# Optimization experiments

Measured on AMD Instinct MI355X. Metric: run time of the kernel, lower is better.

## Reference

```python
import jax, jax.numpy as jnp
import numpy as np

HEAD_SIZE = 64
NUM_HEADS = 8
D_IN = 512

def setup_inputs() -> dict:
    key = jax.random.key(0)
    ks = jax.random.split(key, 6)
    B, Nq, Nk = 4, 2048, 2048
    HD = HEAD_SIZE * NUM_HEADS
    q = jax.random.normal(ks[0], (B, Nq, D_IN), dtype=jnp.float32)
    k = jax.random.normal(ks[1], (B, Nk, D_IN), dtype=jnp.float32)
    s = 1.0 / np.sqrt(D_IN)
    Wq = jax.random.normal(ks[2], (D_IN, HD), dtype=jnp.float32) * s
    Wk = jax.random.normal(ks[3], (D_IN, HD), dtype=jnp.float32) * s
    Wv = jax.random.normal(ks[4], (D_IN, HD), dtype=jnp.float32) * s
    Wh = jax.random.normal(ks[5], (HD, HEAD_SIZE), dtype=jnp.float32) * (1.0 / np.sqrt(HD))
    return {"q": q, "k": k, "Wq": Wq, "Wk": Wk, "Wv": Wv, "Wh": Wh}

def reference(q, k, Wq, Wk, Wv, Wh):
    B, Nq, _ = q.shape
    Nk = k.shape[1]
    H, hs = NUM_HEADS, HEAD_SIZE
    # QKV projections (no bias), reshape to [B, H, N, hs]
    q_ = (q @ Wq).reshape(B, Nq, H, hs).transpose(0, 2, 1, 3)
    k_ = (k @ Wk).reshape(B, Nk, H, hs).transpose(0, 2, 1, 3)
    v_ = (k @ Wv).reshape(B, Nk, H, hs).transpose(0, 2, 1, 3)
    scale = 1.0 / jnp.sqrt(jnp.float32(hs))
    score = jnp.einsum('bhqd,bhkd->bhqk', q_, k_) * scale  # [B,H,Nq,Nk]
    attn = jax.nn.softmax(score, axis=-1)
    wv = jnp.einsum('bhqk,bhkd->bhqd', attn, v_)  # [B,H,Nq,hs]
    wv = wv.transpose(0, 2, 1, 3).reshape(B, Nq, H * hs)
    return wv @ Wh  # [B, Nq, hs]
```

## Files before the change

kernel.cpp:

```cpp
#include <hip/hip_runtime.h>
#include <hip/hip_bf16.h>

#define BB   4
#define NQ   2048
#define NKK  2048
#define DIN  512
#define NH   8
#define HS   64
#define HD   512

typedef __hip_bfloat16 bf16;
typedef unsigned short ushort_t;
typedef __attribute__((ext_vector_type(8))) short short8;
typedef __attribute__((ext_vector_type(4))) float f32x4;
typedef __attribute__((ext_vector_type(16))) float f32x16;
typedef __attribute__((ext_vector_type(4))) unsigned u32x4;

__device__ __forceinline__ unsigned short f2bu(float x) {
  bf16 h = __float2bfloat16(x);
  return *(unsigned short*)&h;
}

__global__ __launch_bounds__(256) void wtrans_kernel(
    const float* __restrict__ Wq, const float* __restrict__ Wk,
    const float* __restrict__ Wv, const float* __restrict__ Wh,
    ushort_t* __restrict__ Wt, ushort_t* __restrict__ Wht) {
  const int z = blockIdx.z;
  const float* src;
  ushort_t* dst;
  int S;
  if (z < 3) {
    src = (z == 0) ? Wq : (z == 1) ? Wk : Wv;
    dst = Wt + (size_t)z * 512 * 512;
    S = 512;
  } else {
    if (blockIdx.y != 0) return;
    src = Wh;
    dst = Wht;
    S = 64;
  }
  const int k0 = blockIdx.x * 64;
  const int n0 = (z < 3) ? blockIdx.y * 64 : 0;

  __shared__ ushort_t Ls[64 * 72];
  const int tid = threadIdx.x;
  {
    int r = tid >> 2, cb = (tid & 3) * 16;
    const float* sp = src + (size_t)(k0 + r) * S + n0 + cb;
#pragma unroll
    for (int ii = 0; ii < 4; ++ii) {
      float4 f = *(const float4*)(sp + ii * 4);
      __align__(8) ushort_t t4[4] = {f2bu(f.x), f2bu(f.y), f2bu(f.z), f2bu(f.w)};
      *(uint2*)(&Ls[r * 72 + cb + ii * 4]) = *(uint2*)t4;
    }
  }
  __syncthreads();
  {
    int rr = tid >> 2, tb = (tid & 3) * 16;
    __align__(16) ushort_t tmp[16];
#pragma unroll
    for (int j = 0; j < 16; ++j) tmp[j] = Ls[(tb + j) * 72 + rr];
    ushort_t* dp = dst + (size_t)(n0 + rr) * 512 + k0 + tb;
    *(int4*)dp       = ((int4*)tmp)[0];
    *(int4*)(dp + 8) = ((int4*)tmp)[1];
  }
}

__global__ __launch_bounds__(256) void proj_kernel(
    const float* __restrict__ q, const float* __restrict__ k,
    const ushort_t* __restrict__ Wt, ushort_t* __restrict__ Qf,
    ushort_t* __restrict__ Kf, ushort_t* __restrict__ Vf) {
  const int z = blockIdx.z;
  const float* X = (z == 0) ? q : k;
  const ushort_t* Wz = Wt + (size_t)z * 512 * 512;
  ushort_t* Y = (z == 0) ? Qf : (z == 1) ? Kf : Vf;
  const float sc = (z == 0) ? 0.18033688011112042f : 1.0f;

  __shared__ ushort_t As[2 * 128 * 40];
  __shared__ ushort_t Bs[2 * 128 * 40];

  const int tid  = threadIdx.x;
  const int lane = tid & 63;
  const int w    = tid >> 6;
  const int quad = lane >> 4;
  const int c    = lane & 15;
  const int wm   = w >> 1, wn = w & 1;

  const int m0 = blockIdx.y * 128;
  const int n0 = blockIdx.x * 128;
  const int sm  = tid >> 1;
  const int skb = (tid & 1) * 16;

  float4 xa[4];
  int4 wb[2];
  auto load_t = [&](int k0) {
    const float* xp = X + (size_t)(m0 + sm) * DIN + k0 + skb;
    xa[0] = *(const float4*)(xp + 0);
    xa[1] = *(const float4*)(xp + 4);
    xa[2] = *(const float4*)(xp + 8);
    xa[3] = *(const float4*)(xp + 12);
    const ushort_t* wp = Wz + (size_t)(n0 + sm) * 512 + k0 + skb;
    wb[0] = *(const int4*)wp;
    wb[1] = *(const int4*)(wp + 8);
  };
  auto store_t = [&](int buf) {
    __align__(16) ushort_t ta[16];
#pragma unroll
    for (int ii = 0; ii < 4; ++ii) {
      ta[ii * 4 + 0] = f2bu(xa[ii].x);
      ta[ii * 4 + 1] = f2bu(xa[ii].y);
      ta[ii * 4 + 2] = f2bu(xa[ii].z);
      ta[ii * 4 + 3] = f2bu(xa[ii].w);
    }
    *(int4*)(&As[buf * 5120 + sm * 40 + skb])     = ((int4*)ta)[0];
    *(int4*)(&As[buf * 5120 + sm * 40 + skb + 8]) = ((int4*)ta)[1];
    *(int4*)(&Bs[buf * 5120 + sm * 40 + skb])     = wb[0];
    *(int4*)(&Bs[buf * 5120 + sm * 40 + skb + 8]) = wb[1];
  };

  f32x4 acc[4][4];
#pragma unroll
  for (int m = 0; m < 4; ++m)
#pragma unroll
    for (int n = 0; n < 4; ++n) acc[m][n] = (f32x4)0.0f;

  load_t(0);
  store_t(0);
  __syncthreads();

  for (int t = 0; t < 16; ++t) {
    const int cur = t & 1;
    if (t < 15) load_t((t + 1) * 32);
    const ushort_t* as = As + cur * 5120;
    const ushort_t* bs = Bs + cur * 5120;
    short8 af[4], bfr[4];
#pragma unroll
    for (int m = 0; m < 4; ++m)
      af[m] = *(const short8*)(&as[(wm * 64 + m * 16 + c) * 40 + quad * 8]);
#pragma unroll
    for (int n = 0; n < 4; ++n)
      bfr[n] = *(const short8*)(&bs[(wn * 64 + n * 16 + c) * 40 + quad * 8]);
#pragma unroll
    for (int m = 0; m < 4; ++m)
#pragma unroll
      for (int n = 0; n < 4; ++n)
        acc[m][n] = __builtin_amdgcn_mfma_f32_16x16x32_bf16(af[m], bfr[n], acc[m][n], 0, 0, 0);
    if (t < 15) store_t(cur ^ 1);
    __syncthreads();
  }

#pragma unroll
  for (int m = 0; m < 4; ++m)
#pragma unroll
    for (int n = 0; n < 4; ++n)
#pragma unroll
      for (int r = 0; r < 4; ++r) {
        int row = m0 + wm * 64 + m * 16 + quad * 4 + r;
        int col = n0 + wn * 64 + n * 16 + c;
        Y[(size_t)row * HD + col] = f2bu(acc[m][n][r] * sc);
      }
}

__global__ __launch_bounds__(256) void vtrans_kernel(
    const ushort_t* __restrict__ Vf, ushort_t* __restrict__ Vt) {
  const int b  = blockIdx.z;
  const int t0 = blockIdx.x * 64;
  const int c0 = blockIdx.y * 64;
  __shared__ ushort_t Ls[64 * 72];
  const int tid = threadIdx.x;
  {
    int r = tid >> 2, cb = (tid & 3) * 16;
    const ushort_t* src = Vf + (size_t)(b * NQ + t0 + r) * HD + c0 + cb;
    *(int4*)(&Ls[r * 72 + cb])     = *(const int4*)src;
    *(int4*)(&Ls[r * 72 + cb + 8]) = *(const int4*)(src + 8);
  }
  __syncthreads();
  {
    int rr = tid >> 2, tb = (tid & 3) * 16;
    __align__(16) ushort_t tmp[16];
#pragma unroll
    for (int j = 0; j < 16; ++j) tmp[j] = Ls[(tb + j) * 72 + rr];
    ushort_t* dst = Vt + (size_t)(b * HD + c0 + rr) * NKK + t0 + tb;
    *(int4*)dst       = ((int4*)tmp)[0];
    *(int4*)(dst + 8) = ((int4*)tmp)[1];
  }
}

__global__ __launch_bounds__(128) void attn_kernel(
    const ushort_t* __restrict__ Qf, const ushort_t* __restrict__ Kf,
    const ushort_t* __restrict__ Vt, ushort_t* __restrict__ CTX) {
  const int id   = blockIdx.x;
  const int xcd  = id & 7;
  const int slot = id >> 3;
  const int p    = xcd * 4 + (slot >> 4);
  const int qb   = slot & 15;
  const int h    = p & 7;
  const int b    = p >> 3;

  __shared__ ushort_t Kt[2 * 64 * 64];
  __shared__ ushort_t Vs[2 * 64 * 64];

  const int tid  = threadIdx.x;
  const int lane = tid & 63;
  const int w    = tid >> 6;
  const int ql   = lane & 31;
  const int hi   = lane >> 5;

  const int q0 = qb * 128 + w * 64;

  short8 bq[2][4];
#pragma unroll
  for (int qs = 0; qs < 2; ++qs) {
    const ushort_t* qp =
        Qf + (size_t)(b * NQ + q0 + qs * 32 + ql) * HD + h * HS + hi * 8;
#pragma unroll
    for (int ks = 0; ks < 4; ++ks) bq[qs][ks] = *(const short8*)(qp + ks * 16);
  }

  const int sub  = lane >> 3;
  const int slt  = lane & 7;
  const int csrc = slt ^ sub;
  const ushort_t* kp0 =
      Kf + (size_t)(b * NKK + w * 32 + sub) * HD + h * HS + csrc * 8;
  const ushort_t* vp0 =
      Vt + (size_t)((b * NH + h) * HS + w * 32 + sub) * NKK + csrc * 8;

  auto stage = [&](int buf, int kt) {
    const ushort_t* kp = kp0 + (size_t)kt * 64 * HD;
    const ushort_t* vp = vp0 + (size_t)kt * 64;
#pragma unroll
    for (int i = 0; i < 4; ++i) {
      __builtin_amdgcn_global_load_lds(
          (const __attribute__((address_space(1))) unsigned*)(kp + (size_t)i * 8 * HD),
          (__attribute__((address_space(3))) unsigned*)(&Kt[buf * 4096 + (w * 4 + i) * 512]),
          16, 0, 0);
      __builtin_amdgcn_global_load_lds(
          (const __attribute__((address_space(1))) unsigned*)(vp + (size_t)i * 8 * NKK),
          (__attribute__((address_space(3))) unsigned*)(&Vs[buf * 4096 + (w * 4 + i) * 512]),
          16, 0, 0);
    }
  };

  f32x16 o[2][2];
#pragma unroll
  for (int qs = 0; qs < 2; ++qs)
#pragma unroll
    for (int ng = 0; ng < 2; ++ng) o[qs][ng] = (f32x16)0.0f;
  float lsum[2] = {0.0f, 0.0f};

  stage(0, 0);
  __syncthreads();

  for (int kt = 0; kt < NKK / 64; ++kt) {
    const int cur = kt & 1;
    if (kt < NKK / 64 - 1) stage(cur ^ 1, kt + 1);
    const ushort_t* kb = &Kt[cur * 4096];
    const ushort_t* vb = &Vs[cur * 4096];

#pragma unroll
    for (int kg = 0; kg < 2; ++kg) {
      f32x16 s[2];
      s[0] = (f32x16)0.0f;
      s[1] = (f32x16)0.0f;
      const int krow = kg * 32 + ql;
      __builtin_amdgcn_s_setprio(1);
#pragma unroll
      for (int ks = 0; ks < 4; ++ks) {
        short8 ak = *(const short8*)(&kb[krow * 64 + (((ks * 2 + hi) ^ (krow & 7)) * 8)]);
        s[0] = __builtin_amdgcn_mfma_f32_32x32x16_bf16(ak, bq[0][ks], s[0], 0, 0, 0);
        s[1] = __builtin_amdgcn_mfma_f32_32x32x16_bf16(ak, bq[1][ks], s[1], 0, 0, 0);
      }
      __builtin_amdgcn_s_setprio(0);

      short8 pa[2][2];
#pragma unroll
      for (int qs = 0; qs < 2; ++qs) {
        float p_[16];
#pragma unroll
        for (int r = 0; r < 16; ++r) p_[r] = __builtin_amdgcn_exp2f(s[qs][r]);
        {
          float a0 = p_[0] + p_[1], a1 = p_[2] + p_[3], a2 = p_[4] + p_[5], a3 = p_[6] + p_[7];
          float a4 = p_[8] + p_[9], a5 = p_[10] + p_[11], a6 = p_[12] + p_[13], a7 = p_[14] + p_[15];
          a0 += a1; a2 += a3; a4 += a5; a6 += a7;
          lsum[qs] += (a0 + a2) + (a4 + a6);
        }
#pragma unroll
        for (int sp = 0; sp < 2; ++sp) {
          unsigned wA, wB, wC, wD;
          asm("v_cvt_pk_bf16_f32 %0, %1, %2" : "=v"(wA) : "v"(p_[8 * sp + 0]), "v"(p_[8 * sp + 1]));
          asm("v_cvt_pk_bf16_f32 %0, %1, %2" : "=v"(wB) : "v"(p_[8 * sp + 2]), "v"(p_[8 * sp + 3]));
          asm("v_cvt_pk_bf16_f32 %0, %1, %2" : "=v"(wC) : "v"(p_[8 * sp + 4]), "v"(p_[8 * sp + 5]));
          asm("v_cvt_pk_bf16_f32 %0, %1, %2" : "=v"(wD) : "v"(p_[8 * sp + 6]), "v"(p_[8 * sp + 7]));
          asm("v_permlane32_swap_b32 %0, %1" : "+v"(wA), "+v"(wC));
          asm("v_permlane32_swap_b32 %0, %1" : "+v"(wB), "+v"(wD));
          u32x4 pw;
          pw.x = wA;
          pw.y = wB;
          pw.z = wC;
          pw.w = wD;
          pa[qs][sp] = __builtin_bit_cast(short8, pw);
        }
      }

      __builtin_amdgcn_s_setprio(1);
#pragma unroll
      for (int sp = 0; sp < 2; ++sp) {
        const int ks = kg * 2 + sp;
#pragma unroll
        for (int ng = 0; ng < 2; ++ng) {
          const int vrow = ng * 32 + ql;
          short8 bv = *(const short8*)(&vb[vrow * 64 + (((ks * 2 + hi) ^ (vrow & 7)) * 8)]);
          o[0][ng] = __builtin_amdgcn_mfma_f32_32x32x16_bf16(pa[0][sp], bv, o[0][ng], 0, 0, 0);
          o[1][ng] = __builtin_amdgcn_mfma_f32_32x32x16_bf16(pa[1][sp], bv, o[1][ng], 0, 0, 0);
        }
      }
      __builtin_amdgcn_s_setprio(0);
    }

    __syncthreads();
  }

  float inv[2];
#pragma unroll
  for (int qs = 0; qs < 2; ++qs) {
    float tot = lsum[qs] + __shfl_xor(lsum[qs], 32);
    inv[qs] = 1.0f / tot;
  }

#pragma unroll
  for (int qs = 0; qs < 2; ++qs)
#pragma unroll
    for (int r = 0; r < 16; ++r) {
      int qr = (r & 3) + 8 * (r >> 2) + 4 * hi;
      float iv = __shfl(inv[qs], qr);
      size_t base = (size_t)(b * NQ + q0 + qs * 32 + qr) * HD + h * HS + ql;
      CTX[base]      = f2bu(o[qs][0][r] * iv);
      CTX[base + 32] = f2bu(o[qs][1][r] * iv);
    }
}

__global__ __launch_bounds__(64) void outproj_kernel(
    const ushort_t* __restrict__ CTX, const ushort_t* __restrict__ Wht,
    float* __restrict__ out) {
  const int lane = threadIdx.x & 63;
  const int quad = lane >> 4, c = lane & 15;
  const int m0 = blockIdx.x * 16;

  f32x4 o[4];
#pragma unroll
  for (int n = 0; n < 4; ++n) o[n] = (f32x4)0.0f;

  const ushort_t* arow = CTX + (size_t)(m0 + c) * HD;
#pragma unroll 4
  for (int ks = 0; ks < 16; ++ks) {
    short8 a = *(const short8*)(arow + ks * 32 + quad * 8);
#pragma unroll
    for (int nd = 0; nd < 4; ++nd) {
      short8 bn = *(const short8*)(Wht + (size_t)(nd * 16 + c) * 512 + ks * 32 + quad * 8);
      o[nd] = __builtin_amdgcn_mfma_f32_16x16x32_bf16(a, bn, o[nd], 0, 0, 0);
    }
  }
#pragma unroll
  for (int nd = 0; nd < 4; ++nd)
#pragma unroll
    for (int r = 0; r < 4; ++r)
      out[(size_t)(m0 + quad * 4 + r) * HS + nd * 16 + c] = o[nd][r];
}

extern "C" void kernel_launch(void* const* d_in, const int* in_sizes, int n_in,
                              void* d_out, int out_size, void* d_ws,
                              size_t ws_size, hipStream_t stream) {
  const float* q  = (const float*)d_in[0];
  const float* k  = (const float*)d_in[1];
  const float* Wq = (const float*)d_in[2];
  const float* Wk = (const float*)d_in[3];
  const float* Wv = (const float*)d_in[4];
  const float* Wh = (const float*)d_in[5];
  float* out = (float*)d_out;

  const size_t E = (size_t)BB * NQ * HD;
  ushort_t* ws  = (ushort_t*)d_ws;
  ushort_t* Qf  = ws;
  ushort_t* Kf  = Qf + E;
  ushort_t* Vt  = Kf + E;
  ushort_t* CTX = Vt + E;
  ushort_t* Vf  = CTX + E;
  ushort_t* Wt  = Vf + E;
  ushort_t* Wht = Wt + (size_t)3 * 512 * 512;

  wtrans_kernel<<<dim3(8, 8, 4), 256, 0, stream>>>(Wq, Wk, Wv, Wh, Wt, Wht);
  proj_kernel<<<dim3(HD / 128, BB * NQ / 128, 3), 256, 0, stream>>>(
      q, k, Wt, Qf, Kf, Vf);
  vtrans_kernel<<<dim3(NKK / 64, HD / 64, BB), 256, 0, stream>>>(Vf, Vt);
  attn_kernel<<<dim3(16 * NH * BB), 128, 0, stream>>>(Qf, Kf, Vt, CTX);
  outproj_kernel<<<dim3(BB * NQ / 16), 64, 0, stream>>>(CTX, Wht, out);
}
```

Measured before the change: 197.3 us.

## Make attention one wave per block and drop barriers with explicit vmcnt waits

The attention kernel drops from two waves per block to one wave per block, and the grid doubles to 1024 blocks. Each wave now stages the whole 64-row K/V tile into its own double buffer. `__syncthreads` is replaced by `s_waitcnt vmcnt` on the async global-to-LDS loads. All K and V fragments for a tile are also loaded from LDS into registers up front, before the MFMA chains. This removes barrier stalls and the intra-block coupling. In exchange, K/V are no longer shared between two waves, so global/L2 traffic doubles, and register pressure rises from the preloaded fragments.

After: 199.1 us. About the same (+0.9%).

```diff
diff --git a/kernel.cpp b/kernel.cpp
--- a/kernel.cpp
+++ b/kernel.cpp
@@ -186,27 +186,25 @@
   }
 }
 
-__global__ __launch_bounds__(128) void attn_kernel(
+__global__ __launch_bounds__(64, 1) void attn_kernel(
     const ushort_t* __restrict__ Qf, const ushort_t* __restrict__ Kf,
     const ushort_t* __restrict__ Vt, ushort_t* __restrict__ CTX) {
   const int id   = blockIdx.x;
   const int xcd  = id & 7;
   const int slot = id >> 3;
-  const int p    = xcd * 4 + (slot >> 4);
-  const int qb   = slot & 15;
+  const int p    = xcd * 4 + (slot >> 5);
+  const int qb   = slot & 31;
   const int h    = p & 7;
   const int b    = p >> 3;
 
-  __shared__ ushort_t Kt[2 * 64 * 64];
-  __shared__ ushort_t Vs[2 * 64 * 64];
-
-  const int tid  = threadIdx.x;
-  const int lane = tid & 63;
-  const int w    = tid >> 6;
+  __shared__ ushort_t Kt[2][4096];
+  __shared__ ushort_t Vs[2][4096];
+
+  const int lane = threadIdx.x & 63;
   const int ql   = lane & 31;
   const int hi   = lane >> 5;
 
-  const int q0 = qb * 128 + w * 64;
+  const int q0 = qb * 64;
 
   short8 bq[2][4];
 #pragma unroll
@@ -221,22 +219,22 @@
   const int slt  = lane & 7;
   const int csrc = slt ^ sub;
   const ushort_t* kp0 =
-      Kf + (size_t)(b * NKK + w * 32 + sub) * HD + h * HS + csrc * 8;
+      Kf + (size_t)(b * NKK + sub) * HD + h * HS + csrc * 8;
   const ushort_t* vp0 =
-      Vt + (size_t)((b * NH + h) * HS + w * 32 + sub) * NKK + csrc * 8;
+      Vt + (size_t)((b * NH + h) * HS + sub) * NKK + csrc * 8;
 
   auto stage = [&](int buf, int kt) {
     const ushort_t* kp = kp0 + (size_t)kt * 64 * HD;
     const ushort_t* vp = vp0 + (size_t)kt * 64;
 #pragma unroll
-    for (int i = 0; i < 4; ++i) {
+    for (int i = 0; i < 8; ++i) {
       __builtin_amdgcn_global_load_lds(
           (const __attribute__((address_space(1))) unsigned*)(kp + (size_t)i * 8 * HD),
-          (__attribute__((address_space(3))) unsigned*)(&Kt[buf * 4096 + (w * 4 + i) * 512]),
+          (__attribute__((address_space(3))) unsigned*)(&Kt[buf][i * 512]),
           16, 0, 0);
       __builtin_amdgcn_global_load_lds(
           (const __attribute__((address_space(1))) unsigned*)(vp + (size_t)i * 8 * NKK),
-          (__attribute__((address_space(3))) unsigned*)(&Vs[buf * 4096 + (w * 4 + i) * 512]),
+          (__attribute__((address_space(3))) unsigned*)(&Vs[buf][i * 512]),
           16, 0, 0);
     }
   };
@@ -249,26 +247,44 @@
   float lsum[2] = {0.0f, 0.0f};
 
   stage(0, 0);
-  __syncthreads();
-
-  for (int kt = 0; kt < NKK / 64; ++kt) {
-    const int cur = kt & 1;
-    if (kt < NKK / 64 - 1) stage(cur ^ 1, kt + 1);
-    const ushort_t* kb = &Kt[cur * 4096];
-    const ushort_t* vb = &Vs[cur * 4096];
+
+  for (int t = 0; t < NKK / 64; ++t) {
+    const int buf = t & 1;
+    if (t < NKK / 64 - 1) {
+      stage(buf ^ 1, t + 1);
+      asm volatile("s_waitcnt vmcnt(16)" ::: "memory");
+    } else {
+      asm volatile("s_waitcnt vmcnt(0)" ::: "memory");
+    }
+    const ushort_t* kb = &Kt[buf][0];
+    const ushort_t* vb = &Vs[buf][0];
+
+    short8 ak[2][4], bv[2][4];
+#pragma unroll
+    for (int kg = 0; kg < 2; ++kg) {
+      const int krow = kg * 32 + ql;
+#pragma unroll
+      for (int ks = 0; ks < 4; ++ks)
+        ak[kg][ks] = *(const short8*)(&kb[krow * 64 + (((ks * 2 + hi) ^ (krow & 7)) * 8)]);
+    }
+#pragma unroll
+    for (int ng = 0; ng < 2; ++ng) {
+      const int vrow = ng * 32 + ql;
+#pragma unroll
+      for (int ks = 0; ks < 4; ++ks)
+        bv[ng][ks] = *(const short8*)(&vb[vrow * 64 + (((ks * 2 + hi) ^ (vrow & 7)) * 8)]);
+    }
 
 #pragma unroll
     for (int kg = 0; kg < 2; ++kg) {
       f32x16 s[2];
       s[0] = (f32x16)0.0f;
       s[1] = (f32x16)0.0f;
-      const int krow = kg * 32 + ql;
       __builtin_amdgcn_s_setprio(1);
 #pragma unroll
       for (int ks = 0; ks < 4; ++ks) {
-        short8 ak = *(const short8*)(&kb[krow * 64 + (((ks * 2 + hi) ^ (krow & 7)) * 8)]);
-        s[0] = __builtin_amdgcn_mfma_f32_32x32x16_bf16(ak, bq[0][ks], s[0], 0, 0, 0);
-        s[1] = __builtin_amdgcn_mfma_f32_32x32x16_bf16(ak, bq[1][ks], s[1], 0, 0, 0);
+        s[0] = __builtin_amdgcn_mfma_f32_32x32x16_bf16(ak[kg][ks], bq[0][ks], s[0], 0, 0, 0);
+        s[1] = __builtin_amdgcn_mfma_f32_32x32x16_bf16(ak[kg][ks], bq[1][ks], s[1], 0, 0, 0);
       }
       __builtin_amdgcn_s_setprio(0);
 
@@ -308,16 +324,12 @@
         const int ks = kg * 2 + sp;
 #pragma unroll
         for (int ng = 0; ng < 2; ++ng) {
-          const int vrow = ng * 32 + ql;
-          short8 bv = *(const short8*)(&vb[vrow * 64 + (((ks * 2 + hi) ^ (vrow & 7)) * 8)]);
-          o[0][ng] = __builtin_amdgcn_mfma_f32_32x32x16_bf16(pa[0][sp], bv, o[0][ng], 0, 0, 0);
-          o[1][ng] = __builtin_amdgcn_mfma_f32_32x32x16_bf16(pa[1][sp], bv, o[1][ng], 0, 0, 0);
+          o[0][ng] = __builtin_amdgcn_mfma_f32_32x32x16_bf16(pa[0][sp], bv[ng][ks], o[0][ng], 0, 0, 0);
+          o[1][ng] = __builtin_amdgcn_mfma_f32_32x32x16_bf16(pa[1][sp], bv[ng][ks], o[1][ng], 0, 0, 0);
         }
       }
       __builtin_amdgcn_s_setprio(0);
     }
-
-    __syncthreads();
   }
 
   float inv[2];
@@ -392,6 +404,6 @@
   proj_kernel<<<dim3(HD / 128, BB * NQ / 128, 3), 256, 0, stream>>>(
       q, k, Wt, Qf, Kf, Vf);
   vtrans_kernel<<<dim3(NKK / 64, HD / 64, BB), 256, 0, stream>>>(Vf, Vt);
-  attn_kernel<<<dim3(16 * NH * BB), 128, 0, stream>>>(Qf, Kf, Vt, CTX);
+  attn_kernel<<<dim3(32 * NH * BB), 64, 0, stream>>>(Qf, Kf, Vt, CTX);
   outproj_kernel<<<dim3(BB * NQ / 16), 64, 0, stream>>>(CTX, Wht, out);
 }
```
